# Performance work log

Measured on AMD Instinct MI355X. Metric: run time of the kernel, lower is better.

Reference implementation:

```python
import jax, jax.numpy as jnp
import numpy as np

EPS = 1e-6
NUM_HEADS = 12


def ln_cf(x, w, b):
    # channels_first LayerNorm over channel dim (ConvNeXt style)
    u = jnp.mean(x, axis=1, keepdims=True)
    s = jnp.mean((x - u) ** 2, axis=1, keepdims=True)
    xn = (x - u) / jnp.sqrt(s + EPS)
    shp = (1, -1) + (1,) * (x.ndim - 2)
    return xn * w.reshape(shp) + b.reshape(shp)


def conv2s2(x, w):
    # Conv3d kernel=2 stride=2 (no bias): exact non-overlapping patch contraction
    b, c, H, W, D = x.shape
    xp = x.reshape(b, c, H // 2, 2, W // 2, 2, D // 2, 2)
    return jnp.einsum('bchkwpdq,ockpq->bohwd', xp, w)


def convt2s2(x, w):
    # ConvTranspose3d kernel=2 stride=2 (torch weight layout [in, out, 2,2,2])
    b, i, H, W, D = x.shape
    o = w.shape[1]
    y = jnp.einsum('bihwd,iokpq->bohkwpdq', x, w)
    return y.reshape(b, o, 2 * H, 2 * W, 2 * D)


def stem(x, w1, g1, b1, w2, g2, b2):
    h = conv2s2(x, w1)
    h = jax.nn.gelu(ln_cf(h, g1, b1), approximate=False)
    h = conv2s2(h, w2)
    return ln_cf(h, g2, b2)


def debed(x, tw1, g, b, tw2, tb2):
    h = convt2s2(x, tw1)
    h = jax.nn.gelu(ln_cf(h, g, b), approximate=False)
    return convt2s2(h, tw2) + tb2.reshape(1, -1, 1, 1, 1)


def rope(x):
    # rotary embedding over full token dim c (pairs (i, i+c/2)), positions 0..L-1
    b, l, c = x.shape
    inv = 1.0 / (10000.0 ** (jnp.arange(0, c, 2, dtype=jnp.float32) / c))
    t = jnp.arange(l, dtype=jnp.float32)
    f = jnp.outer(t, inv)                      # [l, c/2]
    emb = jnp.concatenate([f, f], axis=-1)     # [l, c]
    cos, sin = jnp.cos(emb)[None], jnp.sin(emb)[None]
    rot = jnp.concatenate([-x[..., c // 2:], x[..., :c // 2]], axis=-1)
    return x * cos + rot * sin


def _forward(x, skip, q_w1, q_g1, q_b1, q_w2, q_g2, q_b2,
             k_w1, k_g1, k_b1, k_w2, k_g2, k_b2,
             v_w1, v_g1, v_b1, v_w2, v_g2, v_b2,
             o_tw1, o_g, o_b, o_tw2, o_tb2,
             ns_w, ns_b, nx_w, nx_b, no_w, no_b):
    res = skip
    skip = ln_cf(skip, ns_w, ns_b)
    x = ln_cf(x, nx_w, nx_b)
    q = stem(skip, q_w1, q_g1, q_b1, q_w2, q_g2, q_b2)
    k = stem(x, k_w1, k_g1, k_b1, k_w2, k_g2, k_b2)
    v = stem(x, v_w1, v_g1, v_b1, v_w2, v_g2, v_b2)
    b, c, Hq, Wq, Dq = q.shape
    _, _, Hk, Wk, Dk = k.shape
    q = q.reshape(b, c, -1).transpose(0, 2, 1)   # [b, Lq, c]
    k = k.reshape(b, c, -1).transpose(0, 2, 1)   # [b, Lk, c]
    v = v.reshape(b, c, -1).transpose(0, 2, 1)
    q = rope(q)
    k = rope(k)
    hd = c // NUM_HEADS
    qh = q.reshape(b, -1, NUM_HEADS, hd).transpose(0, 2, 1, 3)  # [b, nh, Lq, hd]
    kh = k.reshape(b, -1, NUM_HEADS, hd).transpose(0, 2, 1, 3)
    vh = v.reshape(b, -1, NUM_HEADS, hd).transpose(0, 2, 1, 3)
    scale = 1.0 / jnp.sqrt(jnp.float32(hd))
    attn = jax.nn.softmax(jnp.einsum('bhqc,bhkc->bhqk', qh, kh) * scale, axis=-1)
    proj = jnp.einsum('bhqk,bhkc->bhqc', attn, vh)              # [b, nh, Lq, hd]
    # rearrange 'b nh l c -> b (c nh) h w d'
    proj = proj.transpose(0, 3, 1, 2).reshape(b, c, Hq, Wq, Dq)
    proj = ln_cf(proj, no_w, no_b)
    out = debed(proj, o_tw1, o_g, o_b, o_tw2, o_tb2)
    return out + res


def setup_inputs() -> dict:
    key = jax.random.key(0)
    ks = iter(jax.random.split(key, 40))
    def nrm(shape, scale):
        return jax.random.normal(next(ks), shape, jnp.float32) * scale
    E, E4, XF, SF = 768, 192, 6, 6
    inp = {
        'x': nrm((2, XF, 48, 48, 48), 1.0),
        'skip': nrm((2, SF, 48, 48, 48), 1.0),
    }
    for p, ic in [('q', SF), ('k', XF), ('v', XF)]:
        inp[p + '_w1'] = nrm((E4, ic, 2, 2, 2), (ic * 8) ** -0.5)
        inp[p + '_g1'] = jnp.ones(E4, jnp.float32)
        inp[p + '_b1'] = jnp.zeros(E4, jnp.float32)
        inp[p + '_w2'] = nrm((E, E4, 2, 2, 2), (E4 * 8) ** -0.5)
        inp[p + '_g2'] = jnp.ones(E, jnp.float32)
        inp[p + '_b2'] = jnp.zeros(E, jnp.float32)
    inp['o_tw1'] = nrm((E, E4, 2, 2, 2), E ** -0.5)
    inp['o_g'] = jnp.ones(E4, jnp.float32)
    inp['o_b'] = jnp.zeros(E4, jnp.float32)
    inp['o_tw2'] = nrm((E4, SF, 2, 2, 2), E4 ** -0.5)
    inp['o_tb2'] = jnp.zeros(SF, jnp.float32)
    inp['ns_w'] = jnp.ones(SF, jnp.float32)
    inp['ns_b'] = jnp.zeros(SF, jnp.float32)
    inp['nx_w'] = jnp.ones(XF, jnp.float32)
    inp['nx_b'] = jnp.zeros(XF, jnp.float32)
    inp['no_w'] = jnp.ones(E, jnp.float32)
    inp['no_b'] = jnp.zeros(E, jnp.float32)
    return inp


def reference(x, skip, q_w1, q_g1, q_b1, q_w2, q_g2, q_b2,
              k_w1, k_g1, k_b1, k_w2, k_g2, k_b2,
              v_w1, v_g1, v_b1, v_w2, v_g2, v_b2,
              o_tw1, o_g, o_b, o_tw2, o_tb2,
              ns_w, ns_b, nx_w, nx_b, no_w, no_b):
    return _forward(x, skip, q_w1, q_g1, q_b1, q_w2, q_g2, q_b2,
                    k_w1, k_g1, k_b1, k_w2, k_g2, k_b2,
                    v_w1, v_g1, v_b1, v_w2, v_g2, v_b2,
                    o_tw1, o_g, o_b, o_tw2, o_tb2,
                    ns_w, ns_b, nx_w, nx_b, no_w, no_b)
```

## Files before the change

kernel.cpp:

```cpp
#include <hip/hip_runtime.h>
#include <math.h>

#define BB_ 2
#define C0 6
#define S0 48
#define V0 (S0*S0*S0)
#define C1 192
#define S1 24
#define V1 (S1*S1*S1)
#define C2 768
#define S2 12
#define LL (S2*S2*S2)
#define NH 12
#define HD 64
#define KDIM (C1*8)
#define MDIM (BB_*LL)

typedef __attribute__((ext_vector_type(8))) short short8;
typedef __attribute__((ext_vector_type(4))) short short4v;
typedef __attribute__((ext_vector_type(4))) float float4v;

static __device__ __forceinline__ float gelu_exact(float x){
  return 0.5f*x*(1.0f+erff(x*0.70710678118654752440f));
}
static __device__ __forceinline__ unsigned short f2bf(float f){
  unsigned int u = __float_as_uint(f);
  unsigned int r = (u + 0x7fffu + ((u>>16)&1u)) >> 16;
  return (unsigned short)r;
}
static __device__ __forceinline__ unsigned int pk_bf16(float a, float b){
#if __has_builtin(__builtin_amdgcn_cvt_pk_bf16_f32)
  typedef __attribute__((ext_vector_type(2))) __bf16 bf2;
  bf2 r = __builtin_amdgcn_cvt_pk_bf16_f32(a,b);
  union { bf2 v; unsigned int u; } cv; cv.v = r;
  return cv.u;
#else
  return (unsigned int)f2bf(a) | ((unsigned int)f2bf(b)<<16);
#endif
}
static __device__ __forceinline__ float bf2f(unsigned short u){
  return __uint_as_float(((unsigned int)u)<<16);
}
static __device__ __forceinline__ void load_lds16(const void* g, void* l){
  __builtin_amdgcn_global_load_lds((const __attribute__((address_space(1))) unsigned int*)g,
      (__attribute__((address_space(3))) unsigned int*)l, 16, 0, 0);
}
static __device__ __forceinline__ float4v mfma32(short8 a, short8 b, float4v c){
  return __builtin_amdgcn_mfma_f32_16x16x32_bf16(a,b,c,0,0,0);
}
static __device__ __forceinline__ float4v mfma16(short4v a, short4v b, float4v c){
#if __has_builtin(__builtin_amdgcn_mfma_f32_16x16x16bf16_1k)
  return __builtin_amdgcn_mfma_f32_16x16x16bf16_1k(a,b,c,0,0,0);
#else
  asm volatile("v_mfma_f32_16x16x16_bf16 %0, %1, %2, %0" : "+v"(c) : "v"(a), "v"(b));
  return c;
#endif
}

__global__ __launch_bounds__(256) void prep_kernel(
    const float* __restrict__ skin, const float* __restrict__ xin,
    const float* __restrict__ nsw, const float* __restrict__ nsb,
    const float* __restrict__ nxw, const float* __restrict__ nxb,
    unsigned short* __restrict__ outS, unsigned short* __restrict__ outX,
    const float* __restrict__ qw2, const float* __restrict__ kw2, const float* __restrict__ vw2,
    const float* __restrict__ tw1, const float* __restrict__ tw2,
    const float* __restrict__ qw1, const float* __restrict__ kw1, const float* __restrict__ vw1,
    unsigned short* __restrict__ w2tq, unsigned short* __restrict__ w2tk,
    unsigned short* __restrict__ w2tv, unsigned short* __restrict__ Btd,
    unsigned short* __restrict__ Bt48,
    unsigned short* __restrict__ w1q, unsigned short* __restrict__ w1k,
    unsigned short* __restrict__ w1v){
  int bx = blockIdx.x;
  if (bx < 1728){
    int z = bx >= 864;
    const float* in = z ? xin : skin;
    const float* w  = z ? nxw : nsw;
    const float* bi = z ? nxb : nsb;
    unsigned short* out = z ? outX : outS;
    int idx = (bx - z*864)*256 + threadIdx.x;
    int b = idx / V0, vox = idx - b*V0;
    const float* p = in + (size_t)b*(C0*V0) + vox;
    float v[C0]; float s=0.f;
#pragma unroll
    for (int c=0;c<C0;c++){ v[c]=p[(size_t)c*V0]; s+=v[c]; }
    float u = s*(1.f/C0);
    float ss=0.f;
#pragma unroll
    for (int c=0;c<C0;c++){ float d=v[c]-u; ss+=d*d; }
    float inv = rsqrtf(ss*(1.f/C0)+1e-6f);
    unsigned short* o = out + (size_t)b*(C0*V0) + vox;
#pragma unroll
    for (int c=0;c<C0;c++) o[(size_t)c*V0] = f2bf((v[c]-u)*inv*w[c]+bi[c]);
    return;
  }
  bx -= 1728;
  if (bx < 13824){
    int z = bx/4608;
    int idx = (bx - z*4608)*256 + threadIdx.x;
    const float* w2 = (z==0)?qw2:((z==1)?kw2:vw2);
    unsigned short* o = (z==0)?w2tq:((z==1)?w2tk:w2tv);
    int oc = idx/KDIM; int r = idx-oc*KDIM; int p = r/C1; int ic = r-p*C1;
    o[idx] = f2bf(w2[(size_t)oc*KDIM + ic*8 + p]);
  } else if (bx < 18432){
    int idx = (bx-13824)*256 + threadIdx.x;
    int n = idx/C2; int p = idx-n*C2;
    int i = ((p&63)*NH) + (p>>6);
    int kpq = n/C1, o2 = n-kpq*C1;
    Btd[idx] = f2bf(tw1[(size_t)i*KDIM + o2*8 + kpq]);
  } else if (bx < 18480){
    int idx = (bx-18432)*256 + threadIdx.x;
    int n = idx/C1; int i = idx-n*C1;
    Bt48[idx] = (n<48) ? f2bf(tw2[(size_t)i*48 + n]) : (unsigned short)0;
  } else {
    int idx = (bx-18480)*256 + threadIdx.x;
    int z = idx / 9216; int r = idx - z*9216;
    const float* w1 = (z==0)?qw1:((z==1)?kw1:vw1);
    unsigned short* o = (z==0)?w1q:((z==1)?w1k:w1v);
    o[r] = f2bf(w1[r]);
  }
}

__global__ __launch_bounds__(256) void conv1_kernel(
    const unsigned short* __restrict__ lnSb, const unsigned short* __restrict__ lnXb,
    const unsigned short* __restrict__ w1bq, const unsigned short* __restrict__ w1bk,
    const unsigned short* __restrict__ w1bv,
    const float* __restrict__ qg1, const float* __restrict__ qb1,
    const float* __restrict__ kg1, const float* __restrict__ kb1,
    const float* __restrict__ vg1, const float* __restrict__ vb1,
    unsigned short* __restrict__ h1q, unsigned short* __restrict__ h1k,
    unsigned short* __restrict__ h1v){
  int z = blockIdx.z;
  const unsigned short* in = (z==0)? lnSb : lnXb;
  const unsigned short* Wb = (z==0)?w1bq:((z==1)?w1bk:w1bv);
  const float* g1 = (z==0)?qg1:((z==1)?kg1:vg1);
  const float* b1 = (z==0)?qb1:((z==1)?kb1:vb1);
  unsigned short* h1p = (z==0)?h1q:((z==1)?h1k:h1v);
  int t = threadIdx.x, w = t>>6, lane = t&63;
  int g = lane>>4, l16 = lane&15;
  int j = blockIdx.x*4 + w;
  int bxh = j/18, mt = j - bxh*18;
  int b = bxh/48; int rem = bxh - b*48; int y = rem>>1, xh = rem&1;
  int xo = mt/3, zo = mt - xo*3;
  int xv = xh*12 + xo*2 + (l16>>3);
  int zv = zo*8 + (l16&7);
  int x2 = 2*xv, z2 = 2*zv, y2 = 2*y;
  const unsigned short* base = in + (size_t)b*C0*V0;
  union { short8 v; unsigned int u[4]; } aA;
  {
    size_t rb = (size_t)g*V0;
    aA.u[0] = *(const unsigned int*)&base[rb + (y2+0)*(S0*S0) + (x2+0)*S0 + z2];
    aA.u[1] = *(const unsigned int*)&base[rb + (y2+0)*(S0*S0) + (x2+1)*S0 + z2];
    aA.u[2] = *(const unsigned int*)&base[rb + (y2+1)*(S0*S0) + (x2+0)*S0 + z2];
    aA.u[3] = *(const unsigned int*)&base[rb + (y2+1)*(S0*S0) + (x2+1)*S0 + z2];
  }
  union { short4v v; unsigned int u[2]; } aB;
  {
    size_t rb = (size_t)(4+(g>>1))*V0 + (y2+(g&1))*(S0*S0);
    aB.u[0] = *(const unsigned int*)&base[rb + (x2+0)*S0 + z2];
    aB.u[1] = *(const unsigned int*)&base[rb + (x2+1)*S0 + z2];
  }
  float4v acc[12];
#pragma unroll
  for (int ot=0; ot<12; ot++){
    short8  wA = *(const short8*)&Wb[(ot*16+l16)*48 + g*8];
    short4v wB = *(const short4v*)&Wb[(ot*16+l16)*48 + 32 + g*4];
    float4v a = {};
    a = mfma32(wA, aA.v, a);
    a = mfma16(wB, aB.v, a);
    acc[ot] = a;
  }
  float s1=0.f, s2=0.f;
#pragma unroll
  for (int ot=0;ot<12;ot++)
#pragma unroll
    for (int reg=0;reg<4;reg++){ float v=acc[ot][reg]; s1+=v; s2+=v*v; }
  s1 += __shfl_xor(s1,16); s1 += __shfl_xor(s1,32);
  s2 += __shfl_xor(s2,16); s2 += __shfl_xor(s2,32);
  float u = s1*(1.f/C1);
  float inv = rsqrtf(s2*(1.f/C1)-u*u+1e-6f);
  int tok = (y>>1)*(S2*S2) + (xv>>1)*S2 + (zv>>1);
  int p8 = (y&1)*4 + (xv&1)*2 + (zv&1);
  unsigned short* hb = h1p + (size_t)(b*LL+tok)*KDIM + p8*C1;
#pragma unroll
  for (int ot=0; ot<12; ot++){
    int oc0 = ot*16 + g*4;
    float4 gg = *(const float4*)&g1[oc0];
    float4 bb = *(const float4*)&b1[oc0];
    float x0 = gelu_exact((acc[ot][0]-u)*inv*gg.x+bb.x);
    float x1 = gelu_exact((acc[ot][1]-u)*inv*gg.y+bb.y);
    float x2e= gelu_exact((acc[ot][2]-u)*inv*gg.z+bb.z);
    float x3 = gelu_exact((acc[ot][3]-u)*inv*gg.w+bb.w);
    uint2 pk; pk.x = pk_bf16(x0,x1); pk.y = pk_bf16(x2e,x3);
    *(uint2*)&hb[oc0] = pk;
  }
}

__global__ __launch_bounds__(256) void gemm_stem_kernel(
    const unsigned short* __restrict__ A0, const unsigned short* __restrict__ A1,
    const unsigned short* __restrict__ A2,
    const unsigned short* __restrict__ B0, const unsigned short* __restrict__ B1,
    const unsigned short* __restrict__ B2,
    unsigned short* __restrict__ Cq, unsigned short* __restrict__ Ck,
    unsigned short* __restrict__ Cv){
  int flat = blockIdx.x;
  int xcd = flat & 7, slot = flat >> 3;
  int tile = xcd*61 + slot;
  if (tile >= 486) return;
  int z = tile/162; int rr = tile - z*162;
  int m0 = (rr/6)*128, n0 = (rr - (rr/6)*6)*128;
  const unsigned short* A = (z==0)?A0:((z==1)?A1:A2);
  const unsigned short* Bt = (z==0)?B0:((z==1)?B1:B2);
  unsigned short* Cp = (z==0)?Cq:((z==1)?Ck:Cv);
  __shared__ __align__(16) unsigned short Al[2][128*32];
  __shared__ __align__(16) unsigned short Bl[2][128*32];
  int t=threadIdx.x, w=t>>6, lane=t&63;
  int g=lane>>4, l16=lane&15, r16=lane>>2, c16=lane&3;
  int wm=w>>1, wn=w&1;
  float4v acc[4][4] = {};
#pragma unroll
  for (int cc=0;cc<4;cc++){
    int ch = w*4+cc;
    if (ch<8){
      const unsigned short* gp = A + (size_t)(m0+ch*16+r16)*KDIM + 0 + c16*8;
      load_lds16(gp, &Al[0][ch*512]);
    } else {
      const unsigned short* gp = Bt + (size_t)(n0+(ch-8)*16+r16)*KDIM + 0 + c16*8;
      load_lds16(gp, &Bl[0][(ch-8)*512]);
    }
  }
  __syncthreads();
  int cur = 0;
  for (int kb=0;kb<KDIM;kb+=32){
    if (kb+32 < KDIM){
      int nb = cur^1;
#pragma unroll
      for (int cc=0;cc<4;cc++){
        int ch = w*4+cc;
        if (ch<8){
          const unsigned short* gp = A + (size_t)(m0+ch*16+r16)*KDIM + (kb+32) + c16*8;
          load_lds16(gp, &Al[nb][ch*512]);
        } else {
          const unsigned short* gp = Bt + (size_t)(n0+(ch-8)*16+r16)*KDIM + (kb+32) + c16*8;
          load_lds16(gp, &Bl[nb][(ch-8)*512]);
        }
      }
    }
    short8 af[4], bf[4];
#pragma unroll
    for (int mt=0;mt<4;mt++) af[mt] = *(const short8*)&Al[cur][(wm*64+mt*16+l16)*32 + g*8];
#pragma unroll
    for (int nt=0;nt<4;nt++) bf[nt] = *(const short8*)&Bl[cur][(wn*64+nt*16+l16)*32 + g*8];
#pragma unroll
    for (int mt=0;mt<4;mt++)
#pragma unroll
      for (int nt=0;nt<4;nt++)
        acc[mt][nt] = mfma32(af[mt], bf[nt], acc[mt][nt]);
    __syncthreads();
    cur ^= 1;
  }
#pragma unroll
  for (int mt=0;mt<4;mt++){
    int mb = m0 + wm*64 + mt*16 + g*4;
#pragma unroll
    for (int nt=0;nt<4;nt++){
      int col = n0 + wn*64 + nt*16 + l16;
#pragma unroll
      for (int reg=0;reg<4;reg++)
        Cp[(size_t)(mb+reg)*C2 + col] = f2bf(acc[mt][nt][reg]);
    }
  }
}

__global__ __launch_bounds__(256) void gemm_debed_kernel(const unsigned short* __restrict__ A,
    const unsigned short* __restrict__ Bt, unsigned short* __restrict__ C){
  int flat = blockIdx.x;
  int xcd = flat & 7, slot = flat >> 3;
  int tile = xcd*41 + slot;
  if (tile >= 324) return;
  int m0 = (tile/12)*128, n0 = (tile - (tile/12)*12)*128;
  __shared__ __align__(16) unsigned short Al[2][128*32];
  __shared__ __align__(16) unsigned short Bl[2][128*32];
  int t=threadIdx.x, w=t>>6, lane=t&63;
  int g=lane>>4, l16=lane&15, r16=lane>>2, c16=lane&3;
  int wm=w>>1, wn=w&1;
  float4v acc[4][4] = {};
#pragma unroll
  for (int cc=0;cc<4;cc++){
    int ch = w*4+cc;
    if (ch<8){
      const unsigned short* gp = A + (size_t)(m0+ch*16+r16)*C2 + 0 + c16*8;
      load_lds16(gp, &Al[0][ch*512]);
    } else {
      const unsigned short* gp = Bt + (size_t)(n0+(ch-8)*16+r16)*C2 + 0 + c16*8;
      load_lds16(gp, &Bl[0][(ch-8)*512]);
    }
  }
  __syncthreads();
  int cur = 0;
  for (int kb=0;kb<C2;kb+=32){
    if (kb+32 < C2){
      int nb = cur^1;
#pragma unroll
      for (int cc=0;cc<4;cc++){
        int ch = w*4+cc;
        if (ch<8){
          const unsigned short* gp = A + (size_t)(m0+ch*16+r16)*C2 + (kb+32) + c16*8;
          load_lds16(gp, &Al[nb][ch*512]);
        } else {
          const unsigned short* gp = Bt + (size_t)(n0+(ch-8)*16+r16)*C2 + (kb+32) + c16*8;
          load_lds16(gp, &Bl[nb][(ch-8)*512]);
        }
      }
    }
    short8 af[4], bf[4];
#pragma unroll
    for (int mt=0;mt<4;mt++) af[mt] = *(const short8*)&Al[cur][(wm*64+mt*16+l16)*32 + g*8];
#pragma unroll
    for (int nt=0;nt<4;nt++) bf[nt] = *(const short8*)&Bl[cur][(wn*64+nt*16+l16)*32 + g*8];
#pragma unroll
    for (int mt=0;mt<4;mt++)
#pragma unroll
      for (int nt=0;nt<4;nt++)
        acc[mt][nt] = mfma32(af[mt], bf[nt], acc[mt][nt]);
    __syncthreads();
    cur ^= 1;
  }
#pragma unroll
  for (int nt=0;nt<4;nt++){
    int n = n0 + wn*64 + nt*16 + l16;
    int kpq = n / C1;
    int o = n - kpq*C1;
#pragma unroll
    for (int mt=0;mt<4;mt++){
      int mb = m0 + wm*64 + mt*16 + g*4;
#pragma unroll
      for (int reg=0;reg<4;reg++){
        int m = mb + reg;
        int b = m / LL; int tok = m - b*LL;
        int h = tok/(S2*S2), ww=(tok/S2)%S2, d=tok%S2;
        int v24 = (2*h+((kpq>>2)&1))*(S1*S1) + (2*ww+((kpq>>1)&1))*S1 + (2*d+(kpq&1));
        C[(size_t)(b*V1+v24)*C1 + o] = f2bf(acc[mt][nt][reg]);
      }
    }
  }
}

__global__ __launch_bounds__(256) void final_kernel(const unsigned short* __restrict__ dh,
    const unsigned short* __restrict__ Bt48, const float* __restrict__ og,
    const float* __restrict__ ob, const float* __restrict__ tb2s,
    const float* __restrict__ skipp, float* __restrict__ out){
  __shared__ __align__(16) unsigned short As[64*200];
  __shared__ __align__(16) unsigned short Bs[64*200];
  int t=threadIdx.x, w=t>>6, lane=t&63;
  int g=lane>>4, l16=lane&15;
  int m0 = blockIdx.x*64;
  for (int n8 = t; n8 < 1536; n8 += 256){
    int n64 = n8/24, kk = (n8 - n64*24)*8;
    uint4 d4 = *(const uint4*)&Bt48[n64*192 + kk];
    *(uint4*)&Bs[n64*200 + kk] = d4;
  }
  float g0=og[lane], g1v=og[lane+64], g2v=og[lane+128];
  float b0=ob[lane], b1v=ob[lane+64], b2v=ob[lane+128];
  for (int rr=0; rr<16; rr++){
    int rl = w*16 + rr;
    const unsigned short* row = dh + (size_t)(m0+rl)*C1;
    float v0=bf2f(row[lane]), v1=bf2f(row[lane+64]), v2=bf2f(row[lane+128]);
    float s1=v0+v1+v2, s2=v0*v0+v1*v1+v2*v2;
#pragma unroll
    for (int off=32;off>0;off>>=1){ s1+=__shfl_xor(s1,off); s2+=__shfl_xor(s2,off); }
    float u=s1*(1.f/C1), inv=rsqrtf(s2*(1.f/C1)-u*u+1e-6f);
    As[rl*200+lane]     = f2bf(gelu_exact((v0-u)*inv*g0+b0));
    As[rl*200+lane+64]  = f2bf(gelu_exact((v1-u)*inv*g1v+b1v));
    As[rl*200+lane+128] = f2bf(gelu_exact((v2-u)*inv*g2v+b2v));
  }
  __syncthreads();
  int wm=w>>1, wn=w&1;
  float4v acc[2][2] = {};
#pragma unroll
  for (int kb=0;kb<192;kb+=32){
    short8 af[2], bf[2];
#pragma unroll
    for (int mt=0;mt<2;mt++) af[mt] = *(const short8*)&As[(wm*32+mt*16+l16)*200 + kb + g*8];
#pragma unroll
    for (int nt=0;nt<2;nt++) bf[nt] = *(const short8*)&Bs[(wn*32+nt*16+l16)*200 + kb + g*8];
#pragma unroll
    for (int mt=0;mt<2;mt++)
#pragma unroll
      for (int nt=0;nt<2;nt++)
        acc[mt][nt] = mfma32(af[mt], bf[nt], acc[mt][nt]);
  }
#pragma unroll
  for (int nt=0;nt<2;nt++){
    int n = wn*32 + nt*16 + l16;
    if (n < 48){
      int c = n>>3, kpq = n&7;
      float bias = tb2s[c];
#pragma unroll
      for (int mt=0;mt<2;mt++){
        int mb = m0 + wm*32 + mt*16 + g*4;
#pragma unroll
        for (int reg=0;reg<4;reg++){
          int m = mb + reg;
          int b = m / V1; int v24 = m - b*V1;
          int y24 = v24/(S1*S1), x24=(v24/S1)%S1, z24=v24%S1;
          int vox = (2*y24+((kpq>>2)&1))*(S0*S0) + (2*x24+((kpq>>1)&1))*S0 + 2*z24+(kpq&1);
          size_t oi = (size_t)(b*C0+c)*V0 + vox;
          out[oi] = acc[mt][nt][reg] + bias + skipp[oi];
        }
      }
    }
  }
}

__global__ __launch_bounds__(64) void ln768_stem_kernel(
    unsigned short* __restrict__ qb, unsigned short* __restrict__ kb2,
    unsigned short* __restrict__ vb,
    const float* __restrict__ qg, const float* __restrict__ qbi,
    const float* __restrict__ kg, const float* __restrict__ kbi,
    const float* __restrict__ vg, const float* __restrict__ vbi, float qscale){
  int z = blockIdx.y;
  unsigned short* buf = (z==0)?qb:((z==1)?kb2:vb);
  const float* g  = (z==0)?qg:((z==1)?kg:vg);
  const float* bia= (z==0)?qbi:((z==1)?kbi:vbi);
  float scale = (z==0)? qscale : 1.0f;
  int tok = blockIdx.x, lane = threadIdx.x;
  unsigned short* row = buf + (size_t)tok*C2;
  float v[12]; float s1=0.f,s2=0.f;
#pragma unroll
  for (int i=0;i<12;i++){ float t=bf2f(row[i*64+lane]); v[i]=t; s1+=t; s2+=t*t; }
#pragma unroll
  for (int off=32;off>0;off>>=1){ s1+=__shfl_xor(s1,off); s2+=__shfl_xor(s2,off); }
  float u=s1*(1.f/C2);
  float inv=rsqrtf(s2*(1.f/C2)-u*u+1e-6f);
  if (z==2){
#pragma unroll
    for (int i=0;i<12;i++){ int j=i*64+lane; row[j]=f2bf((v[i]-u)*inv*g[j]+bia[j]); }
  } else {
    int pos = tok % LL;
#pragma unroll
    for (int i=0;i<6;i++){
      int j=i*64+lane;
      float xn1=(v[i]-u)*inv*g[j]+bia[j];
      float xn2=(v[i+6]-u)*inv*g[j+384]+bia[j+384];
      float fr=(float)pos*__expf(-0.02398526139f*(float)j);
      float cs=cosf(fr), sn=sinf(fr);
      row[j]     = f2bf((xn1*cs - xn2*sn)*scale);
      row[j+384] = f2bf((xn2*cs + xn1*sn)*scale);
    }
  }
}

__global__ __launch_bounds__(256) void vtrans_kernel(const unsigned short* __restrict__ vbf,
    unsigned short* __restrict__ vT){
  __shared__ unsigned short T[64*72];
  int tok0 = blockIdx.x*64;
  int h = blockIdx.y, b = blockIdx.z;
  int t = threadIdx.x;
#pragma unroll
  for (int i=0;i<2;i++){
    int idx = t + i*256;
    int token = idx>>3, dc = idx&7;
    uint4 d4 = *(const uint4*)&vbf[(size_t)(b*LL+tok0+token)*C2 + h*64 + dc*8];
    const unsigned short* s = (const unsigned short*)&d4;
#pragma unroll
    for (int j2=0;j2<8;j2++) T[(dc*8+j2)*72 + token] = s[j2];
  }
  __syncthreads();
  int r = t>>2, seg = t&3;
  unsigned short* dst = vT + (size_t)((b*NH+h)*HD + r)*LL + tok0 + seg*16;
  uint4 o[2];
  unsigned short* os = (unsigned short*)o;
#pragma unroll
  for (int j2=0;j2<16;j2++) os[j2] = T[r*72 + seg*16 + j2];
  *(uint4*)dst = o[0];
  *(uint4*)(dst+8) = o[1];
}

__global__ __launch_bounds__(256) void attn_kernel(const unsigned short* __restrict__ q,
    const unsigned short* __restrict__ k, const unsigned short* __restrict__ vt,
    unsigned short* __restrict__ opart, float* __restrict__ lbuf){
  __shared__ __align__(16) unsigned char smem[32768];
  unsigned short* Ks = (unsigned short*)smem;
  unsigned short* Vs = Ks + 4096;
  int flat = blockIdx.x;
  int xcd = flat & 7, slot = flat >> 3;
  int tile = xcd*324 + slot;
  int h = tile / 216; int rem = tile - h*216;
  int zb = rem / 27, qt = rem - zb*27;
  int b = zb >> 2, split = zb & 3;
  int t=threadIdx.x, w=t>>6, lane=t&63;
  int g=lane>>4, l16=lane&15;
  const unsigned short* qrow = q + (size_t)(b*LL + qt*64 + w*16 + l16)*C2 + h*64;
  short8 qA = *(const short8*)(qrow + g*8);
  short8 qB = *(const short8*)(qrow + 32 + g*8);
  const unsigned short* kbase = k + (size_t)(b*LL)*C2 + h*64;
  const unsigned short* vbase = vt + (size_t)((b*NH+h)*HD)*LL;
  int sub = lane>>3;
  int chs = (lane&7) ^ sub;
  int ktb = split*7, kte = (split==3)? 27 : (split*7+7);
  const unsigned short* gptr[4];
  unsigned short* ldst[4];
  int gstep[4];
#pragma unroll
  for (int cc=0;cc<4;cc++){
    int ii = w*4+cc;
    if (ii<8){
      int key = ktb*64 + ii*8 + sub;
      gptr[cc] = kbase + (size_t)key*C2 + chs*8;
      gstep[cc] = 64*C2;
      ldst[cc] = &Ks[ii*512];
    } else {
      int d = (ii-8)*8 + sub;
      gptr[cc] = vbase + (size_t)d*LL + ktb*64 + chs*8;
      gstep[cc] = 64;
      ldst[cc] = &Vs[(ii-8)*512];
    }
  }
  int sw = l16 & 7;
  const unsigned short* ksrow = &Ks[l16*64 + (g^sw)*8];
  int c2d = (((4+g)^sw) - (g^sw))*8;
  const unsigned short* vsrow = &Vs[l16*64 + (g&1)*4];
  int xk[4];
#pragma unroll
  for (int kc=0;kc<4;kc++) xk[kc] = (((kc*2 + (g>>1)) ^ sw))*8;
  short4v vones;
  vones[0]=vones[1]=vones[2]=vones[3]=(short)0x3F80;
  float4v O4[4] = {};
  float4v Ol = {};
#pragma unroll
  for (int cc=0;cc<4;cc++){
    load_lds16(gptr[cc], ldst[cc]);
    gptr[cc] += gstep[cc];
  }
  __syncthreads();
  int cur = 0;
  for (int kt=ktb; kt<kte; kt++){
    if (kt+1 < kte){
      int so = (cur^1)*8192;
#pragma unroll
      for (int cc=0;cc<4;cc++){
        load_lds16(gptr[cc], ldst[cc]+so);
        gptr[cc] += gstep[cc];
      }
    }
    int co = cur*8192;
    const unsigned short* kr = ksrow + co;
    const unsigned short* vr = vsrow + co;
    float4v sc[4];
#pragma unroll
    for (int nt=0;nt<4;nt++){
      short8 k1 = *(const short8*)(kr + nt*1024);
      short8 k2 = *(const short8*)(kr + nt*1024 + c2d);
      float4v zz = {};
      zz = mfma32(k1, qA, zz);
      zz = mfma32(k2, qB, zz);
      sc[nt] = zz;
    }
#pragma unroll
    for (int nt=0;nt<4;nt++)
#pragma unroll
      for (int reg=0;reg<4;reg++)
        sc[nt][reg] = exp2f(sc[nt][reg]);
#pragma unroll
    for (int kc=0;kc<4;kc++){
      union { short4v v; unsigned int u[2]; } pb;
      pb.u[0] = pk_bf16(sc[kc][0], sc[kc][1]);
      pb.u[1] = pk_bf16(sc[kc][2], sc[kc][3]);
      Ol = mfma16(vones, pb.v, Ol);
      const unsigned short* vp = vr + xk[kc];
#pragma unroll
      for (int dt=0;dt<4;dt++){
        short4v va = *(const short4v*)(vp + dt*1024);
        O4[dt] = mfma16(va, pb.v, O4[dt]);
      }
    }
    __syncthreads();
    cur ^= 1;
  }
  float* Ot = (float*)smem;
  float* ot = Ot + w*1216;
#pragma unroll
  for (int dt=0;dt<4;dt++)
    *(float4*)&ot[l16*76 + dt*16 + g*4] =
        make_float4(O4[dt][0],O4[dt][1],O4[dt][2],O4[dt][3]);
  if (g==0){
    int qi = qt*64 + w*16 + l16;
    lbuf[((size_t)(b*4+split)*NH+h)*LL + qi] = Ol[0];
  }
  __syncthreads();
  int qq = lane>>2, c4 = lane&3;
  unsigned short* orow = opart + (size_t)split*MDIM*C2
              + (size_t)(b*LL + qt*64 + w*16 + qq)*C2 + h*64;
#pragma unroll
  for (int p=0;p<4;p++){
    float4 vv = *(float4*)&ot[qq*76 + p*16 + c4*4];
    uint2 pk; pk.x = pk_bf16(vv.x,vv.y); pk.y = pk_bf16(vv.z,vv.w);
    *(uint2*)&orow[p*16 + c4*4] = pk;
  }
}

__global__ __launch_bounds__(256) void attn_post_kernel(const unsigned short* __restrict__ opart,
    const float* __restrict__ lbuf,
    const float* __restrict__ g, const float* __restrict__ bia,
    unsigned short* __restrict__ aob){
  int t=threadIdx.x, w=t>>6, lane=t&63;
  int m = blockIdx.x*4 + w;
  int b = m / LL, l = m - b*LL;
  const unsigned short* o0 = opart + (size_t)m*C2;
  unsigned short* orow = aob + (size_t)m*C2;
  float vv[12]; float s1=0.f, s2=0.f;
#pragma unroll
  for (int i=0;i<12;i++){
    float ls = 0.f;
#pragma unroll
    for (int s=0;s<4;s++) ls += lbuf[((size_t)(b*4+s)*NH+i)*LL + l];
    float inv = 1.f/ls;
    int j = i*64+lane;
    float val = 0.f;
#pragma unroll
    for (int s=0;s<4;s++) val += bf2f(o0[(size_t)s*MDIM*C2 + j]);
    val *= inv;
    vv[i]=val; s1+=val; s2+=val*val;
  }
#pragma unroll
  for (int off=32;off>0;off>>=1){ s1+=__shfl_xor(s1,off); s2+=__shfl_xor(s2,off); }
  float u=s1*(1.f/C2);
  float invs=rsqrtf(s2*(1.f/C2)-u*u+1e-6f);
#pragma unroll
  for (int i=0;i<12;i++){
    int cj = lane*NH + i;
    orow[i*64+lane] = f2bf((vv[i]-u)*invs*g[cj]+bia[cj]);
  }
}

extern "C" void kernel_launch(void* const* d_in, const int* in_sizes, int n_in,
                              void* d_out, int out_size, void* d_ws, size_t ws_size,
                              hipStream_t stream){
  (void)in_sizes; (void)n_in; (void)out_size; (void)ws_size;
  const float* x    =(const float*)d_in[0];
  const float* skip =(const float*)d_in[1];
  const float* q_w1 =(const float*)d_in[2];
  const float* q_g1 =(const float*)d_in[3];
  const float* q_b1 =(const float*)d_in[4];
  const float* q_w2 =(const float*)d_in[5];
  const float* q_g2 =(const float*)d_in[6];
  const float* q_b2 =(const float*)d_in[7];
  const float* k_w1 =(const float*)d_in[8];
  const float* k_g1 =(const float*)d_in[9];
  const float* k_b1 =(const float*)d_in[10];
  const float* k_w2 =(const float*)d_in[11];
  const float* k_g2 =(const float*)d_in[12];
  const float* k_b2 =(const float*)d_in[13];
  const float* v_w1 =(const float*)d_in[14];
  const float* v_g1 =(const float*)d_in[15];
  const float* v_b1 =(const float*)d_in[16];
  const float* v_w2 =(const float*)d_in[17];
  const float* v_g2 =(const float*)d_in[18];
  const float* v_b2 =(const float*)d_in[19];
  const float* o_tw1=(const float*)d_in[20];
  const float* o_g  =(const float*)d_in[21];
  const float* o_b  =(const float*)d_in[22];
  const float* o_tw2=(const float*)d_in[23];
  const float* o_tb2=(const float*)d_in[24];
  const float* ns_w =(const float*)d_in[25];
  const float* ns_b =(const float*)d_in[26];
  const float* nx_w =(const float*)d_in[27];
  const float* nx_b =(const float*)d_in[28];
  const float* no_w =(const float*)d_in[29];
  const float* no_b =(const float*)d_in[30];
  float* out=(float*)d_out;

  char* W = (char*)d_ws;
  unsigned short* lnSb = (unsigned short*)(W + 0);
  unsigned short* lnXb = (unsigned short*)(W + 2654208);
  unsigned short* h1q  = (unsigned short*)(W + 5308416);
  unsigned short* h1k  = (unsigned short*)(W + 15925248);
  unsigned short* h1v  = (unsigned short*)(W + 26542080);
  unsigned short* w2tq = (unsigned short*)(W + 37158912);
  unsigned short* w2tk = (unsigned short*)(W + 39518208);
  unsigned short* w2tv = (unsigned short*)(W + 41877504);
  unsigned short* qbf  = (unsigned short*)(W + 44236800);
  unsigned short* kbf  = (unsigned short*)(W + 49545216);
  unsigned short* vbf  = (unsigned short*)(W + 54853632);
  unsigned short* vT   = (unsigned short*)(W + 60162048);
  unsigned short* aob  = (unsigned short*)(W + 65470464);
  unsigned short* Btd  = (unsigned short*)(W + 70778880);
  unsigned short* Bt48 = (unsigned short*)(W + 73138176);
  unsigned short* w1q  = (unsigned short*)(W + 73162752);
  unsigned short* w1k  = (unsigned short*)(W + 73181184);
  unsigned short* w1v  = (unsigned short*)(W + 73199616);
  float* lbuf  = (float*)(W + 0);
  unsigned short* opart = (unsigned short*)(W + 5308416);
  unsigned short* dh   = (unsigned short*)(W + 5308416);

  const float QSCALE = 0.125f*1.44269504089f;

  prep_kernel<<<20316,256,0,stream>>>(skip, x, ns_w, ns_b, nx_w, nx_b, lnSb, lnXb,
      q_w2,k_w2,v_w2,o_tw1,o_tw2, q_w1,k_w1,v_w1,
      w2tq,w2tk,w2tv,Btd,Bt48, w1q,w1k,w1v);
  conv1_kernel<<<dim3(432,1,3),256,0,stream>>>(lnSb,lnXb, w1q,w1k,w1v,
      q_g1,q_b1, k_g1,k_b1, v_g1,v_b1, h1q,h1k,h1v);
  gemm_stem_kernel<<<488,256,0,stream>>>(h1q,h1k,h1v,
      w2tq,w2tk,w2tv, qbf,kbf,vbf);
  ln768_stem_kernel<<<dim3(MDIM,3),64,0,stream>>>(qbf,kbf,vbf,
      q_g2,q_b2, k_g2,k_b2, v_g2,v_b2, QSCALE);
  vtrans_kernel<<<dim3(27,12,2),256,0,stream>>>(vbf, vT);
  attn_kernel<<<2592,256,0,stream>>>(qbf, kbf, vT, opart, lbuf);
  attn_post_kernel<<<864,256,0,stream>>>(opart, lbuf, no_w, no_b, aob);
  gemm_debed_kernel<<<328,256,0,stream>>>(aob, Btd, dh);
  final_kernel<<<432,256,0,stream>>>(dh, Bt48, o_g, o_b, o_tb2, skip, out);
}
```

Baseline: 325.3 us.

## Process three query subtiles per wave in attention to reuse K/V tiles

Each attention block now handles 192 queries instead of 64. Every wave holds three 16-row Q fragments and reuses each K/V tile it reads from LDS across all three, so the grid shrinks from 2592 to 864 blocks and the tile index mapping is updated to match. This is meant to cut global and LDS traffic for K/V per query and to amortize the load and barrier overhead per tile. exp2f is also swapped for the hardware exp2 builtin. In exchange, register use per thread rises sharply, which can lower occupancy, and the coarser grid may leave CUs unevenly loaded at the tail.

```diff
diff --git a/kernel.cpp b/kernel.cpp
--- a/kernel.cpp
+++ b/kernel.cpp
@@ -40,6 +40,13 @@
 }
 static __device__ __forceinline__ float bf2f(unsigned short u){
   return __uint_as_float(((unsigned int)u)<<16);
+}
+static __device__ __forceinline__ float exp2v(float x){
+#if __has_builtin(__builtin_amdgcn_exp2f)
+  return __builtin_amdgcn_exp2f(x);
+#else
+  return exp2f(x);
+#endif
 }
 static __device__ __forceinline__ void load_lds16(const void* g, void* l){
   __builtin_amdgcn_global_load_lds((const __attribute__((address_space(1))) unsigned int*)g,
@@ -484,15 +491,19 @@
   unsigned short* Vs = Ks + 4096;
   int flat = blockIdx.x;
   int xcd = flat & 7, slot = flat >> 3;
-  int tile = xcd*324 + slot;
-  int h = tile / 216; int rem = tile - h*216;
-  int zb = rem / 27, qt = rem - zb*27;
+  int tile = xcd*108 + slot;
+  int h = tile / 72; int rem = tile - h*72;
+  int zb = rem / 9, qt = rem - zb*9;
   int b = zb >> 2, split = zb & 3;
   int t=threadIdx.x, w=t>>6, lane=t&63;
   int g=lane>>4, l16=lane&15;
-  const unsigned short* qrow = q + (size_t)(b*LL + qt*64 + w*16 + l16)*C2 + h*64;
-  short8 qA = *(const short8*)(qrow + g*8);
-  short8 qB = *(const short8*)(qrow + 32 + g*8);
+  short8 qA[3], qB[3];
+#pragma unroll
+  for (int j=0;j<3;j++){
+    const unsigned short* qrow = q + (size_t)(b*LL + qt*192 + w*48 + j*16 + l16)*C2 + h*64;
+    qA[j] = *(const short8*)(qrow + g*8);
+    qB[j] = *(const short8*)(qrow + 32 + g*8);
+  }
   const unsigned short* kbase = k + (size_t)(b*LL)*C2 + h*64;
   const unsigned short* vbase = vt + (size_t)((b*NH+h)*HD)*LL;
   int sub = lane>>3;
@@ -525,8 +536,8 @@
   for (int kc=0;kc<4;kc++) xk[kc] = (((kc*2 + (g>>1)) ^ sw))*8;
   short4v vones;
   vones[0]=vones[1]=vones[2]=vones[3]=(short)0x3F80;
-  float4v O4[4] = {};
-  float4v Ol = {};
+  float4v O4[3][4] = {};
+  float4v Ol[3] = {};
 #pragma unroll
   for (int cc=0;cc<4;cc++){
     load_lds16(gptr[cc], ldst[cc]);
@@ -546,32 +557,48 @@
     int co = cur*8192;
     const unsigned short* kr = ksrow + co;
     const unsigned short* vr = vsrow + co;
-    float4v sc[4];
+    float4v sc[3][4];
 #pragma unroll
     for (int nt=0;nt<4;nt++){
       short8 k1 = *(const short8*)(kr + nt*1024);
       short8 k2 = *(const short8*)(kr + nt*1024 + c2d);
-      float4v zz = {};
-      zz = mfma32(k1, qA, zz);
-      zz = mfma32(k2, qB, zz);
-      sc[nt] = zz;
-    }
-#pragma unroll
-    for (int nt=0;nt<4;nt++)
-#pragma unroll
-      for (int reg=0;reg<4;reg++)
-        sc[nt][reg] = exp2f(sc[nt][reg]);
+#pragma unroll
+      for (int j=0;j<3;j++){
+        float4v zz = {};
+        zz = mfma32(k1, qA[j], zz);
+        zz = mfma32(k2, qB[j], zz);
+        sc[j][nt] = zz;
+      }
+    }
+#pragma unroll
+    for (int j=0;j<3;j++)
+#pragma unroll
+      for (int nt=0;nt<4;nt++)
+#pragma unroll
+        for (int reg=0;reg<4;reg++)
+          sc[j][nt][reg] = exp2v(sc[j][nt][reg]);
+    short4v pbs[3][4];
+#pragma unroll
+    for (int j=0;j<3;j++)
+#pragma unroll
+      for (int kc=0;kc<4;kc++){
+        union { short4v v; unsigned int u[2]; } pb;
+        pb.u[0] = pk_bf16(sc[j][kc][0], sc[j][kc][1]);
+        pb.u[1] = pk_bf16(sc[j][kc][2], sc[j][kc][3]);
+        pbs[j][kc] = pb.v;
+      }
 #pragma unroll
     for (int kc=0;kc<4;kc++){
-      union { short4v v; unsigned int u[2]; } pb;
-      pb.u[0] = pk_bf16(sc[kc][0], sc[kc][1]);
-      pb.u[1] = pk_bf16(sc[kc][2], sc[kc][3]);
-      Ol = mfma16(vones, pb.v, Ol);
       const unsigned short* vp = vr + xk[kc];
-#pragma unroll
-      for (int dt=0;dt<4;dt++){
-        short4v va = *(const short4v*)(vp + dt*1024);
-        O4[dt] = mfma16(va, pb.v, O4[dt]);
+      short4v va[4];
+#pragma unroll
+      for (int dt=0;dt<4;dt++) va[dt] = *(const short4v*)(vp + dt*1024);
+#pragma unroll
+      for (int j=0;j<3;j++){
+        Ol[j] = mfma16(vones, pbs[j][kc], Ol[j]);
+#pragma unroll
+        for (int dt=0;dt<4;dt++)
+          O4[j][dt] = mfma16(va[dt], pbs[j][kc], O4[j][dt]);
       }
     }
     __syncthreads();
@@ -579,23 +606,26 @@
   }
   float* Ot = (float*)smem;
   float* ot = Ot + w*1216;
-#pragma unroll
-  for (int dt=0;dt<4;dt++)
-    *(float4*)&ot[l16*76 + dt*16 + g*4] =
-        make_float4(O4[dt][0],O4[dt][1],O4[dt][2],O4[dt][3]);
-  if (g==0){
-    int qi = qt*64 + w*16 + l16;
-    lbuf[((size_t)(b*4+split)*NH+h)*LL + qi] = Ol[0];
-  }
-  __syncthreads();
   int qq = lane>>2, c4 = lane&3;
-  unsigned short* orow = opart + (size_t)split*MDIM*C2
-              + (size_t)(b*LL + qt*64 + w*16 + qq)*C2 + h*64;
-#pragma unroll
-  for (int p=0;p<4;p++){
-    float4 vv = *(float4*)&ot[qq*76 + p*16 + c4*4];
-    uint2 pk; pk.x = pk_bf16(vv.x,vv.y); pk.y = pk_bf16(vv.z,vv.w);
-    *(uint2*)&orow[p*16 + c4*4] = pk;
+#pragma unroll
+  for (int j=0;j<3;j++){
+#pragma unroll
+    for (int dt=0;dt<4;dt++)
+      *(float4*)&ot[l16*76 + dt*16 + g*4] =
+          make_float4(O4[j][dt][0],O4[j][dt][1],O4[j][dt][2],O4[j][dt][3]);
+    if (g==0){
+      int qi = qt*192 + w*48 + j*16 + l16;
+      lbuf[((size_t)(b*4+split)*NH+h)*LL + qi] = Ol[j][0];
+    }
+    unsigned short* orow = opart + (size_t)split*MDIM*C2
+                + (size_t)(b*LL + qt*192 + w*48 + j*16 + qq)*C2 + h*64;
+#pragma unroll
+    for (int p=0;p<4;p++){
+      float4 vv = *(float4*)&ot[qq*76 + p*16 + c4*4];
+      uint2 pk; pk.x = pk_bf16(vv.x,vv.y); pk.y = pk_bf16(vv.z,vv.w);
+      *(uint2*)&orow[p*16 + c4*4] = pk;
+    }
+    __syncthreads();
   }
 }
 
@@ -705,7 +735,7 @@
   ln768_stem_kernel<<<dim3(MDIM,3),64,0,stream>>>(qbf,kbf,vbf,
       q_g2,q_b2, k_g2,k_b2, v_g2,v_b2, QSCALE);
   vtrans_kernel<<<dim3(27,12,2),256,0,stream>>>(vbf, vT);
-  attn_kernel<<<2592,256,0,stream>>>(qbf, kbf, vT, opart, lbuf);
+  attn_kernel<<<864,256,0,stream>>>(qbf, kbf, vT, opart, lbuf);
   attn_post_kernel<<<864,256,0,stream>>>(opart, lbuf, no_w, no_b, aob);
   gemm_debed_kernel<<<328,256,0,stream>>>(aob, Btd, dh);
   final_kernel<<<432,256,0,stream>>>(dh, Bt48, o_g, o_b, o_tb2, skip, out);
```

Result: no change. 325.0 us (-0.1%).
